# Kernel optimization log

Hardware: AMD Instinct MI355X
Metric: run time of the kernel (lower is better)

The kernel has to match this reference:

```python
import jax, jax.numpy as jnp
import numpy as np

M = 65536
INPUT_DIM = 16
OUTPUT_DIM = 64
N = 32          # coordinates transformed by the spline
K = 16          # number of spline bins
MIN_BW = 0.001  # DEFAULT_MIN_BIN_WIDTH
MIN_BH = 0.001  # DEFAULT_MIN_BIN_HEIGHT


def setup_inputs() -> dict:
    key = jax.random.key(0)
    k1, k2, k3, k4 = jax.random.split(key, 4)
    c = jax.random.uniform(k1, (M, INPUT_DIM), jnp.float32)
    z = jax.random.uniform(k2, (M, OUTPUT_DIM), jnp.float32)  # data in [0,1] spline domain
    s_in = OUTPUT_DIM - N + INPUT_DIM  # 48
    s_out = N * (2 * K + 1)            # 1056
    W = jax.random.normal(k3, (s_in, s_out), jnp.float32) * 0.05
    b = jax.random.normal(k4, (s_out,), jnp.float32) * 0.05
    return {"c": c, "z": z, "W": W, "b": b}


def _quadratic_spline(inputs, unnormalized_widths, unnormalized_heights):
    # inputs: [m, n] in [0,1]; unnormalized_widths: [m, n, K]; unnormalized_heights: [m, n, K+1]
    num_bins = unnormalized_widths.shape[-1]

    widths = jax.nn.softmax(unnormalized_widths, axis=-1)
    widths = MIN_BW + (1.0 - MIN_BW * num_bins) * widths

    h = jax.nn.softplus(unnormalized_heights) + 0.001  # [m, n, K+1]
    # (heights have K+1 = num_bins+1 knots, so the 'num_bins-1' padding branch is skipped)
    area = jnp.sum((h[..., :-1] + h[..., 1:]) * 0.5 * widths, axis=-1, keepdims=True)
    heights = h / area
    heights = MIN_BH + (1.0 - MIN_BH) * heights

    cdf = jnp.cumsum((heights[..., :-1] + heights[..., 1:]) * 0.5 * widths, axis=-1)
    cdf = cdf.at[..., -1].set(1.0)
    bin_left_cdf = jnp.pad(cdf, ((0, 0), (0, 0), (1, 0)))  # [m, n, K+1]

    locs = jnp.cumsum(widths, axis=-1).at[..., -1].set(1.0)
    bin_locations = jnp.pad(locs, ((0, 0), (0, 0), (1, 0)))  # [m, n, K+1]

    # nflows torchutils.searchsorted: bump last knot by eps, count knots <= input
    locs_eps = bin_locations.at[..., -1].add(1e-6)
    bin_idx = jnp.sum(inputs[..., None] >= locs_eps, axis=-1) - 1  # [m, n] int

    def gather(arr, idx):
        return jnp.take_along_axis(arr, idx[..., None], axis=-1)[..., 0]

    input_bin_locations = gather(bin_locations, bin_idx)
    input_bin_widths = gather(widths, bin_idx)
    input_left_cdf = gather(bin_left_cdf, bin_idx)
    input_left_heights = gather(heights, bin_idx)
    input_right_heights = gather(heights, bin_idx + 1)

    a = 0.5 * (input_right_heights - input_left_heights) * input_bin_widths
    bq = input_left_heights * input_bin_widths
    cq = input_left_cdf

    alpha = (inputs - input_bin_locations) / input_bin_widths
    outputs = jnp.clip(a * alpha ** 2 + bq * alpha + cq, 0.0, 1.0)
    logabsdet = jnp.log(alpha * (input_right_heights - input_left_heights) + input_left_heights)
    return outputs, logabsdet


def reference(c, z, W, b):
    # forward (reverse=False) branch of QuadraticsSpline.forward
    z1, z2 = z[:, :N], z[:, N:]
    z2c = jnp.concatenate([z2, c], axis=1)
    y = z2c @ W + b                                  # conditioner s (linear)
    sv = y.reshape(y.shape[0], N, 2 * K + 1)
    unnormalized_heights = sv[..., : K + 1]          # first split chunk (size K+1)
    unnormalized_widths = sv[..., K + 1:]            # second chunk (size K)
    x1, log_det = _quadratic_spline(z1, unnormalized_widths, unnormalized_heights)
    x = jnp.concatenate([z2, x1], axis=1)            # note: original concatenates (x2, x1)
    return x, log_det.sum(axis=1)
```

## Files before the change

kernel.cpp:

```cpp
#include <hip/hip_runtime.h>
#include <hip/hip_bf16.h>
#include <math.h>

#define M_ROWS 65536
#define NSPLINE 32
#define BM 64
#define WROWS 16
#define GROUP 4
#define NITER (NSPLINE / GROUP)
#define YS 34
#define WB_ELEMS (32 * 3 * 2 * 64 * 8)

typedef __attribute__((ext_vector_type(8))) _Float16 half8;
typedef __attribute__((ext_vector_type(4))) float floatx4;

__device__ __forceinline__ float softplus_fast(float t) {
    float u = t * t;
    if (u > 1.21f) return log1pf(__expf(t));
    float p = fmaf(u, -2.6352e-5f, 3.4722222e-4f);
    p = fmaf(u, p, -5.2083333e-3f);
    p = fmaf(u, p, 0.125f);
    p = fmaf(u, p, 0.69314718f);
    return fmaf(t, 0.5f, p);
}

__global__ void pack_W(const float* __restrict__ W, const float* __restrict__ b,
                       _Float16* __restrict__ WH) {
    int idx = blockIdx.x * 256 + threadIdx.x;
    int j    = idx & 7;
    int lane = (idx >> 3) & 63;
    int half = (idx >> 9) & 1;
    int tmp  = idx >> 10;
    int t    = tmp % 3;
    int sp   = tmp / 3;
    int k  = half * 32 + ((lane >> 4) << 3) + j;
    int cl = t * 16 + (lane & 15);
    float v = 0.0f;
    if (cl < 33 && k <= 48) {
        int col = sp * 33 + cl;
        v = (k < 48) ? W[k * 1056 + col] : b[col];
    }
    WH[idx] = (_Float16)v;
}

__global__ void __launch_bounds__(256) fused_kernel(
    const float* __restrict__ z, const float* __restrict__ c,
    const _Float16* __restrict__ WH, float* __restrict__ out)
{
    __shared__ float lds_y[4 * 64 * YS];

    const int tid  = threadIdx.x;
    const int w    = tid >> 6;
    const int lane = tid & 63;
    const int q    = lane >> 4;
    const int cc   = lane & 15;
    const int row_base = blockIdx.x * BM + w * WROWS;
    float* lds_wv = lds_y + w * (64 * YS);

    #pragma unroll
    for (int it = 0; it < 2; ++it) {
        int idx = it * 64 + lane;
        int rr  = row_base + (idx >> 3);
        int v4  = idx & 7;
        float4 val = *(const float4*)(z + (size_t)rr * 64 + 32 + v4 * 4);
        *(float4*)(out + (size_t)rr * 64 + v4 * 4) = val;
    }

    half8 a0, a1;
    {
        const float* zr = z + (size_t)(row_base + cc) * 64 + 32;
        float4 v0 = *(const float4*)(zr + q * 8);
        float4 v1 = *(const float4*)(zr + q * 8 + 4);
        a0[0]=(_Float16)v0.x; a0[1]=(_Float16)v0.y;
        a0[2]=(_Float16)v0.z; a0[3]=(_Float16)v0.w;
        a0[4]=(_Float16)v1.x; a0[5]=(_Float16)v1.y;
        a0[6]=(_Float16)v1.z; a0[7]=(_Float16)v1.w;
        if (q < 2) {
            const float* cr = c + (size_t)(row_base + cc) * 16 + q * 8;
            float4 u0 = *(const float4*)cr;
            float4 u1 = *(const float4*)(cr + 4);
            a1[0]=(_Float16)u0.x; a1[1]=(_Float16)u0.y;
            a1[2]=(_Float16)u0.z; a1[3]=(_Float16)u0.w;
            a1[4]=(_Float16)u1.x; a1[5]=(_Float16)u1.y;
            a1[6]=(_Float16)u1.z; a1[7]=(_Float16)u1.w;
        } else {
            #pragma unroll
            for (int j = 0; j < 8; ++j) a1[j] = (_Float16)0.0f;
            if (q == 2) a1[0] = (_Float16)1.0f;
        }
    }

    float zin[NITER];
    {
        const float* zr = z + (size_t)(row_base + cc) * 64 + q;
        #pragma unroll
        for (int g = 0; g < NITER; ++g) zin[g] = zr[g * 4];
    }

    float ld_acc = 0.0f;

    #pragma unroll 1
    for (int g = 0; g < NITER; ++g) {
        #pragma unroll
        for (int sp = 0; sp < GROUP; ++sp) {
            const int spg = g * GROUP + sp;
            const int task = sp * 16 + cc;
            #pragma unroll
            for (int t = 0; t < 3; ++t) {
                const half8* p = (const half8*)WH + (size_t)(spg * 3 + t) * 128 + lane;
                half8 b0 = p[0];
                half8 b1 = p[64];
                floatx4 acc = {0.f, 0.f, 0.f, 0.f};
                acc = __builtin_amdgcn_mfma_f32_16x16x32_f16(b0, a0, acc, 0, 0, 0);
                acc = __builtin_amdgcn_mfma_f32_16x16x32_f16(b1, a1, acc, 0, 0, 0);
                if (t < 2) {
                    float* dst = lds_wv + task * YS + t * 16 + q * 4;
                    *(float2*)dst       = make_float2(acc[0], acc[1]);
                    *(float2*)(dst + 2) = make_float2(acc[2], acc[3]);
                } else if (q == 0) {
                    lds_wv[task * YS + 32] = acc[0];
                }
            }
        }

        const int n = g * GROUP + q;
        const float* my = lds_wv + lane * YS;
        float pv[33];
        #pragma unroll
        for (int i = 0; i < 16; ++i) {
            float2 v = *(const float2*)(my + 2 * i);
            pv[2 * i] = v.x; pv[2 * i + 1] = v.y;
        }
        pv[32] = my[32];

        const float in = zin[g];

        float wd[16];
        float sew = 0.f;
        #pragma unroll
        for (int i = 0; i < 16; ++i) {
            float e = __expf(pv[17 + i]);
            wd[i] = e; sew += e;
        }
        const float inv_sew = 0.984f / sew;
        #pragma unroll
        for (int i = 0; i < 16; ++i) wd[i] = 0.001f + wd[i] * inv_sew;

        float h[17];
        #pragma unroll
        for (int i = 0; i < 17; ++i)
            h[i] = softplus_fast(pv[i]) + 0.001f;

        float area = 0.f;
        #pragma unroll
        for (int i = 0; i < 16; ++i) area += (h[i] + h[i + 1]) * 0.5f * wd[i];
        const float inv_area = 0.999f / area;
        #pragma unroll
        for (int i = 0; i < 17; ++i) h[i] = 0.001f + h[i] * inv_area;

        float loc = 0.f, cdfl = 0.f;
        float sel_loc = 0.f, sel_w = wd[0], sel_cdf = 0.f;
        float sel_lh = h[0], sel_rh = h[1];
        #pragma unroll
        for (int bn = 1; bn < 16; ++bn) {
            cdfl = fmaf((h[bn - 1] + h[bn]) * 0.5f, wd[bn - 1], cdfl);
            loc += wd[bn - 1];
            if (in >= loc) {
                sel_loc = loc; sel_w = wd[bn]; sel_cdf = cdfl;
                sel_lh = h[bn]; sel_rh = h[bn + 1];
            }
        }

        const float alpha = (in - sel_loc) / sel_w;
        const float dh    = sel_rh - sel_lh;
        float o = ((0.5f * dh * sel_w) * alpha + sel_lh * sel_w) * alpha + sel_cdf;
        o = fminf(fmaxf(o, 0.0f), 1.0f);
        out[(size_t)(row_base + cc) * 64 + 32 + n] = o;
        ld_acc += __logf(fmaf(alpha, dh, sel_lh));
    }

    ld_acc += __shfl_down(ld_acc, 32, 64);
    ld_acc += __shfl_down(ld_acc, 16, 64);
    if (q == 0)
        out[(size_t)M_ROWS * 64 + row_base + cc] = ld_acc;
}

extern "C" void kernel_launch(void* const* d_in, const int* in_sizes, int n_in,
                              void* d_out, int out_size, void* d_ws, size_t ws_size,
                              hipStream_t stream) {
    const float* c = (const float*)d_in[0];
    const float* z = (const float*)d_in[1];
    const float* W = (const float*)d_in[2];
    const float* b = (const float*)d_in[3];
    float* out = (float*)d_out;
    _Float16* WH = (_Float16*)d_ws;

    pack_W<<<WB_ELEMS / 256, 256, 0, stream>>>(W, b, WH);
    fused_kernel<<<M_ROWS / BM, 256, 0, stream>>>(z, c, WH, out);
}
```

Measured before the change: 118.7 us.

## Software-pipeline spline groups so next group's MFMA overlaps current spline math

Restructures the main loop so the MFMA GEMM and LDS writes for group g+1 are issued before the spline evaluation of group g, with the LDS values read into registers ahead of time. The goal is to hide MFMA and weight-load latency behind the transcendental-heavy spline arithmetic. The z1 inputs are now loaded per iteration instead of preloaded into a register array. The t=2 LDS store is made unconditional, with non-zero q lanes writing to a padding slot, which removes a branch.

```diff
diff --git a/kernel.cpp b/kernel.cpp
--- a/kernel.cpp
+++ b/kernel.cpp
@@ -42,6 +42,88 @@
     }
     WH[idx] = (_Float16)v;
 }
+
+
+#define GEMM_GROUP(GIDX)                                                      \
+    {                                                                         \
+      _Pragma("unroll")                                                       \
+      for (int sp = 0; sp < GROUP; ++sp) {                                    \
+        const int spg = (GIDX) * GROUP + sp;                                  \
+        const int task = sp * 16 + cc;                                        \
+        _Pragma("unroll")                                                     \
+        for (int t = 0; t < 3; ++t) {                                         \
+          const half8* p = (const half8*)WH + (size_t)(spg * 3 + t) * 128 + lane; \
+          half8 b0 = p[0];                                                    \
+          half8 b1 = p[64];                                                   \
+          floatx4 acc = {0.f, 0.f, 0.f, 0.f};                                 \
+          acc = __builtin_amdgcn_mfma_f32_16x16x32_f16(b0, a0, acc, 0, 0, 0); \
+          acc = __builtin_amdgcn_mfma_f32_16x16x32_f16(b1, a1, acc, 0, 0, 0); \
+          if (t < 2) {                                                        \
+            float* dst = lds_wv + task * YS + t * 16 + q * 4;                 \
+            *(float2*)dst       = make_float2(acc[0], acc[1]);                \
+            *(float2*)(dst + 2) = make_float2(acc[2], acc[3]);                \
+          } else {                                                            \
+             \
+            lds_wv[task * YS + 32 + (q != 0)] = acc[0];                       \
+          }                                                                   \
+        }                                                                     \
+      }                                                                       \
+    }
+
+#define READ_PV()                                                             \
+    {                                                                         \
+      const float* my = lds_wv + lane * YS;                                   \
+      _Pragma("unroll")                                                       \
+      for (int i = 0; i < 16; ++i) {                                          \
+        float2 v = *(const float2*)(my + 2 * i);                              \
+        pv[2 * i] = v.x; pv[2 * i + 1] = v.y;                                 \
+      }                                                                       \
+      pv[32] = my[32];                                                        \
+    }
+
+#define SPLINE(GIDX, INVAL)                                                   \
+    {                                                                         \
+      const int n = (GIDX) * GROUP + q;                                       \
+      const float in = (INVAL);                                               \
+      float wd[16];                                                           \
+      float sew = 0.f;                                                        \
+      _Pragma("unroll")                                                       \
+      for (int i = 0; i < 16; ++i) {                                          \
+        float e = __expf(pv[17 + i]);                                         \
+        wd[i] = e; sew += e;                                                  \
+      }                                                                       \
+      const float inv_sew = 0.984f / sew;            \
+      _Pragma("unroll")                                                       \
+      for (int i = 0; i < 16; ++i) wd[i] = 0.001f + wd[i] * inv_sew;          \
+      float h[17];                                                            \
+      _Pragma("unroll")                                                       \
+      for (int i = 0; i < 17; ++i)                                            \
+        h[i] = softplus_fast(pv[i]) + 0.001f;                                 \
+      float area = 0.f;                                                       \
+      _Pragma("unroll")                                                       \
+      for (int i = 0; i < 16; ++i) area += (h[i] + h[i + 1]) * 0.5f * wd[i];  \
+      const float inv_area = 0.999f / area;            \
+      _Pragma("unroll")                                                       \
+      for (int i = 0; i < 17; ++i) h[i] = 0.001f + h[i] * inv_area;           \
+      float loc = 0.f, cdfl = 0.f;                                            \
+      float sel_loc = 0.f, sel_w = wd[0], sel_cdf = 0.f;                      \
+      float sel_lh = h[0], sel_rh = h[1];                                     \
+      _Pragma("unroll")                                                       \
+      for (int bn = 1; bn < 16; ++bn) {                                       \
+        cdfl = fmaf((h[bn - 1] + h[bn]) * 0.5f, wd[bn - 1], cdfl);            \
+        loc += wd[bn - 1];                                                    \
+        if (in >= loc) {                        \
+          sel_loc = loc; sel_w = wd[bn]; sel_cdf = cdfl;                      \
+          sel_lh = h[bn]; sel_rh = h[bn + 1];                                 \
+        }                                                                     \
+      }                                                                       \
+      const float alpha = (in - sel_loc) / sel_w;                             \
+      const float dh    = sel_rh - sel_lh;                                    \
+      float o = ((0.5f * dh * sel_w) * alpha + sel_lh * sel_w) * alpha + sel_cdf; \
+      o = fminf(fmaxf(o, 0.0f), 1.0f);                                        \
+      out[(size_t)(row_base + cc) * 64 + 32 + n] = o;                         \
+      ld_acc += __logf(fmaf(alpha, dh, sel_lh));                              \
+    }
 
 __global__ void __launch_bounds__(256) fused_kernel(
     const float* __restrict__ z, const float* __restrict__ c,
@@ -90,93 +172,25 @@
         }
     }
 
-    float zin[NITER];
+    const float* z1p = z + (size_t)(row_base + cc) * 64 + q;
+
+    float pv[33];
+
+    GEMM_GROUP(0);
+    READ_PV();
+
+    float ld_acc = 0.0f;
+
+    #pragma unroll 1
+    for (int g = 0; g < NITER - 1; ++g) {
+        const float in_g = z1p[g * 4];
+        GEMM_GROUP(g + 1);
+        SPLINE(g, in_g);
+        READ_PV();
+    }
     {
-        const float* zr = z + (size_t)(row_base + cc) * 64 + q;
-        #pragma unroll
-        for (int g = 0; g < NITER; ++g) zin[g] = zr[g * 4];
-    }
-
-    float ld_acc = 0.0f;
-
-    #pragma unroll 1
-    for (int g = 0; g < NITER; ++g) {
-        #pragma unroll
-        for (int sp = 0; sp < GROUP; ++sp) {
-            const int spg = g * GROUP + sp;
-            const int task = sp * 16 + cc;
-            #pragma unroll
-            for (int t = 0; t < 3; ++t) {
-                const half8* p = (const half8*)WH + (size_t)(spg * 3 + t) * 128 + lane;
-                half8 b0 = p[0];
-                half8 b1 = p[64];
-                floatx4 acc = {0.f, 0.f, 0.f, 0.f};
-                acc = __builtin_amdgcn_mfma_f32_16x16x32_f16(b0, a0, acc, 0, 0, 0);
-                acc = __builtin_amdgcn_mfma_f32_16x16x32_f16(b1, a1, acc, 0, 0, 0);
-                if (t < 2) {
-                    float* dst = lds_wv + task * YS + t * 16 + q * 4;
-                    *(float2*)dst       = make_float2(acc[0], acc[1]);
-                    *(float2*)(dst + 2) = make_float2(acc[2], acc[3]);
-                } else if (q == 0) {
-                    lds_wv[task * YS + 32] = acc[0];
-                }
-            }
-        }
-
-        const int n = g * GROUP + q;
-        const float* my = lds_wv + lane * YS;
-        float pv[33];
-        #pragma unroll
-        for (int i = 0; i < 16; ++i) {
-            float2 v = *(const float2*)(my + 2 * i);
-            pv[2 * i] = v.x; pv[2 * i + 1] = v.y;
-        }
-        pv[32] = my[32];
-
-        const float in = zin[g];
-
-        float wd[16];
-        float sew = 0.f;
-        #pragma unroll
-        for (int i = 0; i < 16; ++i) {
-            float e = __expf(pv[17 + i]);
-            wd[i] = e; sew += e;
-        }
-        const float inv_sew = 0.984f / sew;
-        #pragma unroll
-        for (int i = 0; i < 16; ++i) wd[i] = 0.001f + wd[i] * inv_sew;
-
-        float h[17];
-        #pragma unroll
-        for (int i = 0; i < 17; ++i)
-            h[i] = softplus_fast(pv[i]) + 0.001f;
-
-        float area = 0.f;
-        #pragma unroll
-        for (int i = 0; i < 16; ++i) area += (h[i] + h[i + 1]) * 0.5f * wd[i];
-        const float inv_area = 0.999f / area;
-        #pragma unroll
-        for (int i = 0; i < 17; ++i) h[i] = 0.001f + h[i] * inv_area;
-
-        float loc = 0.f, cdfl = 0.f;
-        float sel_loc = 0.f, sel_w = wd[0], sel_cdf = 0.f;
-        float sel_lh = h[0], sel_rh = h[1];
-        #pragma unroll
-        for (int bn = 1; bn < 16; ++bn) {
-            cdfl = fmaf((h[bn - 1] + h[bn]) * 0.5f, wd[bn - 1], cdfl);
-            loc += wd[bn - 1];
-            if (in >= loc) {
-                sel_loc = loc; sel_w = wd[bn]; sel_cdf = cdfl;
-                sel_lh = h[bn]; sel_rh = h[bn + 1];
-            }
-        }
-
-        const float alpha = (in - sel_loc) / sel_w;
-        const float dh    = sel_rh - sel_lh;
-        float o = ((0.5f * dh * sel_w) * alpha + sel_lh * sel_w) * alpha + sel_cdf;
-        o = fminf(fmaxf(o, 0.0f), 1.0f);
-        out[(size_t)(row_base + cc) * 64 + 32 + n] = o;
-        ld_acc += __logf(fmaf(alpha, dh, sel_lh));
+        const float in_l = z1p[(NITER - 1) * 4];
+        SPLINE(NITER - 1, in_l);
     }
 
     ld_acc += __shfl_down(ld_acc, 32, 64);
```

Measured after the change: 140.1 us. +18.0%, slower.

## Repack spline weights so MFMA outputs land directly in per-lane registers

Applied to the files above, without the earlier changes.

The weight packing is rearranged so each MFMA tile's output rows hold 4 splines times 4 parameters. After 9 MFMA tile pairs, every lane owns all 33 parameters of its spline in accumulator registers, so the LDS staging buffer and its write/read round trip go away. The kernel also swaps the IEEE divisions for hardware reciprocal approximations, adds an occupancy hint to launch bounds, and loads z1 inside the loop instead of preloading it. In exchange, register pressure rises from holding 36 accumulator floats, and the fast reciprocals cost a little precision.

```diff
diff --git a/kernel.cpp b/kernel.cpp
--- a/kernel.cpp
+++ b/kernel.cpp
@@ -8,8 +8,8 @@
 #define WROWS 16
 #define GROUP 4
 #define NITER (NSPLINE / GROUP)
-#define YS 34
-#define WB_ELEMS (32 * 3 * 2 * 64 * 8)
+#define NTILE 9
+#define WB_ELEMS (NITER * NTILE * 2 * 64 * 8)
 
 typedef __attribute__((ext_vector_type(8))) _Float16 half8;
 typedef __attribute__((ext_vector_type(4))) float floatx4;
@@ -30,32 +30,33 @@
     int j    = idx & 7;
     int lane = (idx >> 3) & 63;
     int half = (idx >> 9) & 1;
-    int tmp  = idx >> 10;
-    int t    = tmp % 3;
-    int sp   = tmp / 3;
+    int tile = idx >> 10;
+    int tau  = tile % NTILE;
+    int g    = tile / NTILE;
+    int m  = lane & 15;
     int k  = half * 32 + ((lane >> 4) << 3) + j;
-    int cl = t * 16 + (lane & 15);
+    int spline = g * 4 + (m >> 2);
+    int param  = tau * 4 + (m & 3);
     float v = 0.0f;
-    if (cl < 33 && k <= 48) {
-        int col = sp * 33 + cl;
+    if (param < 33 && k <= 48) {
+        int col = spline * 33 + param;
         v = (k < 48) ? W[k * 1056 + col] : b[col];
     }
     WH[idx] = (_Float16)v;
 }
 
-__global__ void __launch_bounds__(256) fused_kernel(
+#define PV(p) (acc[(p) >> 2][(p) & 3])
+
+__global__ void __launch_bounds__(256, 5) fused_kernel(
     const float* __restrict__ z, const float* __restrict__ c,
     const _Float16* __restrict__ WH, float* __restrict__ out)
 {
-    __shared__ float lds_y[4 * 64 * YS];
-
     const int tid  = threadIdx.x;
     const int w    = tid >> 6;
     const int lane = tid & 63;
     const int q    = lane >> 4;
     const int cc   = lane & 15;
     const int row_base = blockIdx.x * BM + w * WROWS;
-    float* lds_wv = lds_y + w * (64 * YS);
 
     #pragma unroll
     for (int it = 0; it < 2; ++it) {
@@ -90,71 +91,48 @@
         }
     }
 
-    float zin[NITER];
-    {
-        const float* zr = z + (size_t)(row_base + cc) * 64 + q;
-        #pragma unroll
-        for (int g = 0; g < NITER; ++g) zin[g] = zr[g * 4];
-    }
+    const float* z1p = z + (size_t)(row_base + cc) * 64 + q;
 
     float ld_acc = 0.0f;
 
     #pragma unroll 1
     for (int g = 0; g < NITER; ++g) {
+        const float in = z1p[g * 4];
+
+        floatx4 acc[NTILE];
+        const half8* base = (const half8*)WH + (size_t)g * (NTILE * 2 * 64) + lane;
         #pragma unroll
-        for (int sp = 0; sp < GROUP; ++sp) {
-            const int spg = g * GROUP + sp;
-            const int task = sp * 16 + cc;
-            #pragma unroll
-            for (int t = 0; t < 3; ++t) {
-                const half8* p = (const half8*)WH + (size_t)(spg * 3 + t) * 128 + lane;
-                half8 b0 = p[0];
-                half8 b1 = p[64];
-                floatx4 acc = {0.f, 0.f, 0.f, 0.f};
-                acc = __builtin_amdgcn_mfma_f32_16x16x32_f16(b0, a0, acc, 0, 0, 0);
-                acc = __builtin_amdgcn_mfma_f32_16x16x32_f16(b1, a1, acc, 0, 0, 0);
-                if (t < 2) {
-                    float* dst = lds_wv + task * YS + t * 16 + q * 4;
-                    *(float2*)dst       = make_float2(acc[0], acc[1]);
-                    *(float2*)(dst + 2) = make_float2(acc[2], acc[3]);
-                } else if (q == 0) {
-                    lds_wv[task * YS + 32] = acc[0];
-                }
-            }
+        for (int t = 0; t < NTILE; ++t) {
+            half8 w0 = base[(t * 2 + 0) * 64];
+            half8 w1 = base[(t * 2 + 1) * 64];
+            floatx4 a = {0.f, 0.f, 0.f, 0.f};
+            a = __builtin_amdgcn_mfma_f32_16x16x32_f16(w0, a0, a, 0, 0, 0);
+            a = __builtin_amdgcn_mfma_f32_16x16x32_f16(w1, a1, a, 0, 0, 0);
+            acc[t] = a;
         }
 
         const int n = g * GROUP + q;
-        const float* my = lds_wv + lane * YS;
-        float pv[33];
-        #pragma unroll
-        for (int i = 0; i < 16; ++i) {
-            float2 v = *(const float2*)(my + 2 * i);
-            pv[2 * i] = v.x; pv[2 * i + 1] = v.y;
-        }
-        pv[32] = my[32];
-
-        const float in = zin[g];
 
         float wd[16];
         float sew = 0.f;
         #pragma unroll
         for (int i = 0; i < 16; ++i) {
-            float e = __expf(pv[17 + i]);
+            float e = __expf(PV(17 + i));
             wd[i] = e; sew += e;
         }
-        const float inv_sew = 0.984f / sew;
+        const float inv_sew = 0.984f * __builtin_amdgcn_rcpf(sew);
         #pragma unroll
         for (int i = 0; i < 16; ++i) wd[i] = 0.001f + wd[i] * inv_sew;
 
         float h[17];
         #pragma unroll
         for (int i = 0; i < 17; ++i)
-            h[i] = softplus_fast(pv[i]) + 0.001f;
+            h[i] = softplus_fast(PV(i)) + 0.001f;
 
         float area = 0.f;
         #pragma unroll
         for (int i = 0; i < 16; ++i) area += (h[i] + h[i + 1]) * 0.5f * wd[i];
-        const float inv_area = 0.999f / area;
+        const float inv_area = 0.999f * __builtin_amdgcn_rcpf(area);
         #pragma unroll
         for (int i = 0; i < 17; ++i) h[i] = 0.001f + h[i] * inv_area;
 
@@ -171,7 +149,7 @@
             }
         }
 
-        const float alpha = (in - sel_loc) / sel_w;
+        const float alpha = (in - sel_loc) * __builtin_amdgcn_rcpf(sel_w);
         const float dh    = sel_rh - sel_lh;
         float o = ((0.5f * dh * sel_w) * alpha + sel_lh * sel_w) * alpha + sel_cdf;
         o = fminf(fmaxf(o, 0.0f), 1.0f);
```

Result: faster. 111.5 us (-6.0%).
